# Kernel optimization log

Hardware: AMD Instinct MI355X
Metric: run time of the kernel (lower is better)

Reference implementation:

```python
import jax, jax.numpy as jnp
import numpy as np

B, N, C, L, E = 8, 8192, 256, 4, 131072  # graphs, nodes/graph, channels (in=hidden=out), layers, edges/graph


def setup_inputs() -> dict:
    key = jax.random.key(0)
    ks = jax.random.split(key, 9)
    batch_node_tsr = jax.random.normal(ks[0], (B, N, C), jnp.float32)
    edge_index = jax.random.randint(ks[1], (B, 2, E), 0, N, jnp.int32)
    batch_last_node_idx_list = jnp.arange(1, B + 1, dtype=jnp.int32) * N - 1
    s1 = 1.0 / np.sqrt(C)
    s2 = 1.0 / np.sqrt(2 * C)
    # Base GraphConv layers: out = x @ Wr.T + sum_nbr(x) @ Wn.T + b  (all CxC since in=hidden=out)
    base_Wr = jax.random.uniform(ks[2], (L, C, C), jnp.float32, -s1, s1)
    base_Wn = jax.random.uniform(ks[3], (L, C, C), jnp.float32, -s1, s1)
    base_b = jax.random.uniform(ks[4], (L, C), jnp.float32, -s1, s1)
    # Adapter GraphConv layers take concatenated (2C) input
    adapt_Wr = jax.random.uniform(ks[5], (L, C, 2 * C), jnp.float32, -s2, s2)
    adapt_Wn = jax.random.uniform(ks[6], (L, C, 2 * C), jnp.float32, -s2, s2)
    adapt_b = jax.random.uniform(ks[7], (L, C), jnp.float32, -s2, s2)
    return dict(batch_node_tsr=batch_node_tsr, base_Wr=base_Wr, base_Wn=base_Wn,
                base_b=base_b, adapt_Wr=adapt_Wr, adapt_Wn=adapt_Wn, adapt_b=adapt_b,
                edge_index=edge_index, batch_last_node_idx_list=batch_last_node_idx_list)


def reference(batch_node_tsr, base_Wr, base_Wn, base_b, adapt_Wr, adapt_Wn, adapt_b,
              edge_index, batch_last_node_idx_list):
    # Batch graphs PyG-style: offset per-graph node indices into one big graph
    offsets = (jnp.arange(B, dtype=edge_index.dtype) * N)[:, None]  # [B,1]
    src = (edge_index[:, 0, :] + offsets).reshape(-1)  # [B*E]
    dst = (edge_index[:, 1, :] + offsets).reshape(-1)  # [B*E]
    x = batch_node_tsr.reshape(B * N, C)

    def gconv(h, Wr, Wn, b):
        # GraphConv: root transform + sum-aggregated neighbor transform
        agg = jax.ops.segment_sum(h[src], dst, num_segments=B * N)
        return h @ Wr.T + agg @ Wn.T + b

    # Base encoder pass, keeping all latent embeds
    lat = [x]
    for i in range(L):
        lat.append(jax.nn.relu(gconv(lat[-1], base_Wr[i], base_Wn[i], base_b[i])))
    base_batch_embed = lat[-1].reshape(B, N, C)

    # Adapter pass: concat(base_latent[i+1], curr) -> adapter GraphConv -> relu
    curr = x
    for i in range(L):
        curr = jax.nn.relu(gconv(jnp.concatenate([lat[i + 1], curr], axis=-1),
                                 adapt_Wr[i], adapt_Wn[i], adapt_b[i]))
    adapter_batch_embed = curr.reshape(B, N, C)
    return base_batch_embed, adapter_batch_embed
```

## Files before the change

### kernel.cpp

```cpp
#include <hip/hip_runtime.h>

#define B_ 8
#define N_ 8192
#define C_ 256
#define L_ 4
#define E_ 131072
#define BN_ 65536
#define EDGES_ 1048576

typedef __attribute__((ext_vector_type(8))) short short8;
typedef __attribute__((ext_vector_type(4))) float f32x4;

__device__ __forceinline__ unsigned short f2bf(float f){
  unsigned int u = __builtin_bit_cast(unsigned int, f);
  u += 0x7fffu + ((u >> 16) & 1u);
  return (unsigned short)(u >> 16);
}
__device__ __forceinline__ float bf2f(unsigned short h){
  unsigned int u = ((unsigned int)h) << 16;
  return __builtin_bit_cast(float, u);
}

__launch_bounds__(256)
__global__ void cvt_bf16_k(const float* __restrict__ in, unsigned short* __restrict__ out, int n4){
  int t = blockIdx.x * 256 + threadIdx.x;
  if (t >= n4) return;
  float4 v = ((const float4*)in)[t];
  ushort4 o;
  o.x = f2bf(v.x); o.y = f2bf(v.y); o.z = f2bf(v.z); o.w = f2bf(v.w);
  ((ushort4*)out)[t] = o;
}

__launch_bounds__(256)
__global__ void hist_k(const int* __restrict__ ei, int* __restrict__ cnt){
  int t = blockIdx.x * 256 + threadIdx.x;
  int b = t >> 17, e = t & (E_ - 1);
  int dst = ei[b * (2 * E_) + E_ + e];
  atomicAdd(&cnt[(b << 13) + dst], 1);
}

__launch_bounds__(256)
__global__ void scan_k(const int* __restrict__ cnt, int* __restrict__ row_ptr, int* __restrict__ cursor){
  __shared__ int lsum[256];
  int t = threadIdx.x;
  int base = t << 8;
  int s = 0;
  for (int i = 0; i < 256; ++i) s += cnt[base + i];
  lsum[t] = s;
  __syncthreads();
  for (int d = 1; d < 256; d <<= 1){
    int v = (t >= d) ? lsum[t - d] : 0;
    __syncthreads();
    lsum[t] += v;
    __syncthreads();
  }
  int off = lsum[t] - s;
  for (int i = 0; i < 256; ++i){
    row_ptr[base + i] = off;
    cursor[base + i]  = off;
    off += cnt[base + i];
  }
  if (t == 255) row_ptr[BN_] = off;
}

__launch_bounds__(256)
__global__ void scat_k(const int* __restrict__ ei, int* __restrict__ cursor, int* __restrict__ col){
  int t = blockIdx.x * 256 + threadIdx.x;
  int b = t >> 17, e = t & (E_ - 1);
  int src = ei[b * (2 * E_) + e];
  int dst = ei[b * (2 * E_) + E_ + e];
  int pos = atomicAdd(&cursor[(b << 13) + dst], 1);
  col[pos] = (b << 13) + src;
}

__launch_bounds__(256)
__global__ void agg_k(const unsigned short* __restrict__ feat, const int* __restrict__ row_ptr,
                      const int* __restrict__ col, unsigned short* __restrict__ out){
  int w = threadIdx.x >> 6, lane = threadIdx.x & 63;
  int g = blockIdx.x & 7, sblk = blockIdx.x >> 3;
  int node = (g << 13) + (sblk << 2) + w;
  int beg = row_ptr[node], end = row_ptr[node + 1];
  int ch = lane << 2;
  float a0=0,a1=0,a2=0,a3=0,b0=0,b1=0,b2=0,b3=0;
  int e = beg;
  for (; e + 2 <= end; e += 2){
    int s0 = col[e], s1 = col[e + 1];
    ushort4 v0 = *(const ushort4*)(feat + ((size_t)s0 << 8) + ch);
    ushort4 v1 = *(const ushort4*)(feat + ((size_t)s1 << 8) + ch);
    a0 += bf2f(v0.x); a1 += bf2f(v0.y); a2 += bf2f(v0.z); a3 += bf2f(v0.w);
    b0 += bf2f(v1.x); b1 += bf2f(v1.y); b2 += bf2f(v1.z); b3 += bf2f(v1.w);
  }
  if (e < end){
    int s0 = col[e];
    ushort4 v0 = *(const ushort4*)(feat + ((size_t)s0 << 8) + ch);
    a0 += bf2f(v0.x); a1 += bf2f(v0.y); a2 += bf2f(v0.z); a3 += bf2f(v0.w);
  }
  ushort4 o;
  o.x = f2bf(a0 + b0); o.y = f2bf(a1 + b1); o.z = f2bf(a2 + b2); o.w = f2bf(a3 + b3);
  *(ushort4*)(out + ((size_t)node << 8) + ch) = o;
}

__launch_bounds__(256)
__global__ void agg2_k(const unsigned short* __restrict__ fA, const unsigned short* __restrict__ fB,
                       const int* __restrict__ row_ptr, const int* __restrict__ col,
                       unsigned short* __restrict__ oA, unsigned short* __restrict__ oB){
  int w = threadIdx.x >> 6, lane = threadIdx.x & 63;
  int g = blockIdx.x & 7, sblk = blockIdx.x >> 3;
  int node = (g << 13) + (sblk << 2) + w;
  int beg = row_ptr[node], end = row_ptr[node + 1];
  int ch = lane << 2;
  float a0=0,a1=0,a2=0,a3=0, c0=0,c1=0,c2=0,c3=0;
  float a4=0,a5=0,a6=0,a7=0, c4=0,c5=0,c6=0,c7=0;
  int e = beg;
  for (; e + 2 <= end; e += 2){
    int s0 = col[e], s1 = col[e + 1];
    ushort4 va0 = *(const ushort4*)(fA + ((size_t)s0 << 8) + ch);
    ushort4 vb0 = *(const ushort4*)(fB + ((size_t)s0 << 8) + ch);
    ushort4 va1 = *(const ushort4*)(fA + ((size_t)s1 << 8) + ch);
    ushort4 vb1 = *(const ushort4*)(fB + ((size_t)s1 << 8) + ch);
    a0 += bf2f(va0.x); a1 += bf2f(va0.y); a2 += bf2f(va0.z); a3 += bf2f(va0.w);
    c0 += bf2f(vb0.x); c1 += bf2f(vb0.y); c2 += bf2f(vb0.z); c3 += bf2f(vb0.w);
    a4 += bf2f(va1.x); a5 += bf2f(va1.y); a6 += bf2f(va1.z); a7 += bf2f(va1.w);
    c4 += bf2f(vb1.x); c5 += bf2f(vb1.y); c6 += bf2f(vb1.z); c7 += bf2f(vb1.w);
  }
  if (e < end){
    int s0 = col[e];
    ushort4 va0 = *(const ushort4*)(fA + ((size_t)s0 << 8) + ch);
    ushort4 vb0 = *(const ushort4*)(fB + ((size_t)s0 << 8) + ch);
    a0 += bf2f(va0.x); a1 += bf2f(va0.y); a2 += bf2f(va0.z); a3 += bf2f(va0.w);
    c0 += bf2f(vb0.x); c1 += bf2f(vb0.y); c2 += bf2f(vb0.z); c3 += bf2f(vb0.w);
  }
  ushort4 oa, ob;
  oa.x = f2bf(a0 + a4); oa.y = f2bf(a1 + a5); oa.z = f2bf(a2 + a6); oa.w = f2bf(a3 + a7);
  ob.x = f2bf(c0 + c4); ob.y = f2bf(c1 + c5); ob.z = f2bf(c2 + c6); ob.w = f2bf(c3 + c7);
  *(ushort4*)(oA + ((size_t)node << 8) + ch) = oa;
  *(ushort4*)(oB + ((size_t)node << 8) + ch) = ob;
}

#define GLDS16(gp, lp) __builtin_amdgcn_global_load_lds( \
    (const __attribute__((address_space(1))) void*)(gp), \
    (__attribute__((address_space(3))) void*)(lp), 16, 0, 0)

template<int P>
__launch_bounds__(256)
__global__ void gemm_k(const unsigned short* __restrict__ A0, const unsigned short* __restrict__ A1,
                       const unsigned short* __restrict__ A2, const unsigned short* __restrict__ A3,
                       const unsigned short* __restrict__ W0, const unsigned short* __restrict__ W1,
                       const unsigned short* __restrict__ W2, const unsigned short* __restrict__ W3,
                       int ldw, const float* __restrict__ bias,
                       unsigned short* __restrict__ outb, float* __restrict__ outf){
  __shared__ unsigned short lds_u[12288];
  unsigned short* a_t = lds_u;
  unsigned short* b_t = lds_u + 4096;
  const unsigned short* As[4] = {A0, A1, A2, A3};
  const unsigned short* Ws[4] = {W0, W1, W2, W3};
  const int m0 = blockIdx.x << 7;
  const int t = threadIdx.x, lane = t & 63;
  const int w = t >> 6;
  const int lrow = lane & 15, kg = lane >> 4;
  f32x4 acc[2][16] = {};
#pragma unroll
  for (int p = 0; p < P; ++p){
    const unsigned short* A = As[p] + (size_t)m0 * C_;
    const unsigned short* W = Ws[p];
    for (int k0 = 0; k0 < C_; k0 += 32){
#pragma unroll
      for (int c = t; c < 512; c += 256){
        int row = c >> 2, seg = c & 3;
        GLDS16(A + row * C_  + k0 + seg * 8, &a_t[c * 8]);
      }
#pragma unroll
      for (int c = t; c < 1024; c += 256){
        int row = c >> 2, seg = c & 3;
        GLDS16(W + row * ldw + k0 + seg * 8, &b_t[c * 8]);
      }
      __syncthreads();
      short8 af[2];
#pragma unroll
      for (int m = 0; m < 2; ++m)
        af[m] = *(const short8*)&a_t[((w << 5) + (m << 4) + lrow) * 32 + (kg << 3)];
#pragma unroll
      for (int h = 0; h < 2; ++h){
        short8 bfr[8];
#pragma unroll
        for (int n2 = 0; n2 < 8; ++n2)
          bfr[n2] = *(const short8*)&b_t[((h << 7) + (n2 << 4) + lrow) * 32 + (kg << 3)];
#pragma unroll
        for (int m = 0; m < 2; ++m)
#pragma unroll
          for (int n2 = 0; n2 < 8; ++n2)
            acc[m][(h << 3) + n2] =
                __builtin_amdgcn_mfma_f32_16x16x32_bf16(af[m], bfr[n2], acc[m][(h << 3) + n2], 0, 0, 0);
      }
      __syncthreads();
    }
  }
  float bv[16];
#pragma unroll
  for (int n = 0; n < 16; ++n) bv[n] = bias[(n << 4) + lrow];
  unsigned short* ep = lds_u + (w << 11);
#pragma unroll
  for (int m = 0; m < 2; ++m){
    const int gr = m0 + (w << 5) + (m << 4);
    if (outf){
#pragma unroll
      for (int n = 0; n < 16; ++n)
#pragma unroll
        for (int j = 0; j < 4; ++j){
          float v = acc[m][n][j] + bv[n];
          v = v > 0.f ? v : 0.f;
          outf[(size_t)(gr + (kg << 2) + j) * C_ + (n << 4) + lrow] = v;
        }
    }
    if (outb){
#pragma unroll
      for (int h = 0; h < 2; ++h){
#pragma unroll
        for (int n2 = 0; n2 < 8; ++n2){
          int n = (h << 3) + n2;
#pragma unroll
          for (int j = 0; j < 4; ++j){
            float v = acc[m][n][j] + bv[n];
            v = v > 0.f ? v : 0.f;
            ep[((kg << 2) + j) * 128 + (n2 << 4) + lrow] = f2bf(v);
          }
        }
#pragma unroll
        for (int k = 0; k < 4; ++k){
          int r = (lane >> 4) + (k << 2);
          short8 v = *(const short8*)&ep[r * 128 + (lane & 15) * 8];
          *(short8*)&outb[(size_t)(gr + r) * C_ + (h << 7) + (lane & 15) * 8] = v;
        }
      }
    }
  }
}

extern "C" void kernel_launch(void* const* d_in, const int* in_sizes, int n_in,
                              void* d_out, int out_size, void* d_ws, size_t ws_size,
                              hipStream_t stream){
  const float* x_f   = (const float*)d_in[0];
  const float* bWr_f = (const float*)d_in[1];
  const float* bWn_f = (const float*)d_in[2];
  const float* bB    = (const float*)d_in[3];
  const float* aWr_f = (const float*)d_in[4];
  const float* aWn_f = (const float*)d_in[5];
  const float* aB    = (const float*)d_in[6];
  const int*   ei    = (const int*)d_in[7];
  float* out = (float*)d_out;
  (void)in_sizes; (void)n_in; (void)out_size; (void)ws_size;

  char* p = (char*)d_ws;
  const size_t BUF = (size_t)BN_ * C_ * sizeof(unsigned short);
  auto alloc = [&](size_t bytes){ void* r = (void*)p; p += (bytes + 255) & ~(size_t)255; return r; };
  unsigned short* xb   = (unsigned short*)alloc(BUF);
  unsigned short* latA = (unsigned short*)alloc(BUF);
  unsigned short* latB = (unsigned short*)alloc(BUF);
  unsigned short* curA = (unsigned short*)alloc(BUF);
  unsigned short* curB = (unsigned short*)alloc(BUF);
  unsigned short* agg0 = (unsigned short*)alloc(BUF);
  unsigned short* agg1 = (unsigned short*)alloc(BUF);
  unsigned short* wbR  = (unsigned short*)alloc((size_t)L_ * C_ * C_ * 2);
  unsigned short* wbN  = (unsigned short*)alloc((size_t)L_ * C_ * C_ * 2);
  unsigned short* waR  = (unsigned short*)alloc((size_t)L_ * C_ * 2 * C_ * 2);
  unsigned short* waN  = (unsigned short*)alloc((size_t)L_ * C_ * 2 * C_ * 2);
  int* cnt     = (int*)alloc((size_t)BN_ * 4);
  int* row_ptr = (int*)alloc((size_t)(BN_ + 1) * 4);
  int* cursor  = (int*)alloc((size_t)BN_ * 4);
  int* colx    = (int*)alloc((size_t)EDGES_ * 4);

  cvt_bf16_k<<<BN_ * C_ / 4 / 256, 256, 0, stream>>>(x_f, xb, BN_ * C_ / 4);
  cvt_bf16_k<<<L_ * C_ * C_ / 4 / 256, 256, 0, stream>>>(bWr_f, wbR, L_ * C_ * C_ / 4);
  cvt_bf16_k<<<L_ * C_ * C_ / 4 / 256, 256, 0, stream>>>(bWn_f, wbN, L_ * C_ * C_ / 4);
  cvt_bf16_k<<<L_ * C_ * 2 * C_ / 4 / 256, 256, 0, stream>>>(aWr_f, waR, L_ * C_ * 2 * C_ / 4);
  cvt_bf16_k<<<L_ * C_ * 2 * C_ / 4 / 256, 256, 0, stream>>>(aWn_f, waN, L_ * C_ * 2 * C_ / 4);

  hipMemsetAsync(cnt, 0, (size_t)BN_ * 4, stream);
  hist_k<<<EDGES_ / 256, 256, 0, stream>>>(ei, cnt);
  scan_k<<<1, 256, 0, stream>>>(cnt, row_ptr, cursor);
  scat_k<<<EDGES_ / 256, 256, 0, stream>>>(ei, cursor, colx);

  const int AGG_GRID  = BN_ / 4;
  const int GEMM_GRID = BN_ / 128;

  const size_t WB = (size_t)C_ * C_;
  const size_t WA = (size_t)C_ * 2 * C_;

  agg_k<<<AGG_GRID, 256, 0, stream>>>(xb, row_ptr, colx, agg0);
  gemm_k<2><<<GEMM_GRID, 256, 0, stream>>>(xb, agg0, nullptr, nullptr,
      wbR, wbN, nullptr, nullptr, C_, bB, latA, nullptr);
  agg_k<<<AGG_GRID, 256, 0, stream>>>(latA, row_ptr, colx, agg1);
  gemm_k<2><<<GEMM_GRID, 256, 0, stream>>>(latA, agg1, nullptr, nullptr,
      wbR + WB, wbN + WB, nullptr, nullptr, C_, bB + 256, latB, nullptr);
  gemm_k<4><<<GEMM_GRID, 256, 0, stream>>>(latA, xb, agg1, agg0,
      waR, waR + 256, waN, waN + 256, 2 * C_, aB, curA, nullptr);
  agg2_k<<<AGG_GRID, 256, 0, stream>>>(latB, curA, row_ptr, colx, agg1, agg0);
  gemm_k<2><<<GEMM_GRID, 256, 0, stream>>>(latB, agg1, nullptr, nullptr,
      wbR + 2 * WB, wbN + 2 * WB, nullptr, nullptr, C_, bB + 512, latA, nullptr);
  gemm_k<4><<<GEMM_GRID, 256, 0, stream>>>(latB, curA, agg1, agg0,
      waR + WA, waR + WA + 256, waN + WA, waN + WA + 256, 2 * C_, aB + 256, curB, nullptr);
  agg2_k<<<AGG_GRID, 256, 0, stream>>>(latA, curB, row_ptr, colx, agg1, agg0);
  gemm_k<2><<<GEMM_GRID, 256, 0, stream>>>(latA, agg1, nullptr, nullptr,
      wbR + 3 * WB, wbN + 3 * WB, nullptr, nullptr, C_, bB + 768, latB, out);
  gemm_k<4><<<GEMM_GRID, 256, 0, stream>>>(latA, curB, agg1, agg0,
      waR + 2 * WA, waR + 2 * WA + 256, waN + 2 * WA, waN + 2 * WA + 256, 2 * C_, aB + 512, curA, nullptr);
  agg2_k<<<AGG_GRID, 256, 0, stream>>>(latB, curA, row_ptr, colx, agg1, agg0);
  gemm_k<4><<<GEMM_GRID, 256, 0, stream>>>(latB, curA, agg1, agg0,
      waR + 3 * WA, waR + 3 * WA + 256, waN + 3 * WA, waN + 3 * WA + 256, 2 * C_, aB + 768,
      nullptr, out + (size_t)BN_ * C_);
}
```

Baseline: 1.248 ms.

## Double-buffer GEMM LDS tiles, bucket CSR by source range, stage fp32 epilogue

The GEMM now double-buffers its LDS tiles so the next k-slice's global-to-LDS loads overlap MFMA work on the current slice, using one barrier per step. The CSR build keys edges by destination plus a 2-bit source-range bucket, so each node's neighbors are partially sorted by source for better gather locality. The aggregation loops unroll by four. The fp32 output epilogue is staged through LDS to issue coalesced float4 stores. Costs are double the LDS use (lower occupancy), a four-times larger count/scan array handled by a single-block scan, and extra LDS traffic in the epilogue.

```diff
diff --git a/kernel.cpp b/kernel.cpp
--- a/kernel.cpp
+++ b/kernel.cpp
@@ -7,6 +7,7 @@
 #define E_ 131072
 #define BN_ 65536
 #define EDGES_ 1048576
+#define NKEY_ (BN_ * 4)
 
 typedef __attribute__((ext_vector_type(8))) short short8;
 typedef __attribute__((ext_vector_type(4))) float f32x4;
@@ -35,17 +36,21 @@
 __global__ void hist_k(const int* __restrict__ ei, int* __restrict__ cnt){
   int t = blockIdx.x * 256 + threadIdx.x;
   int b = t >> 17, e = t & (E_ - 1);
+  int src = ei[b * (2 * E_) + e];
   int dst = ei[b * (2 * E_) + E_ + e];
-  atomicAdd(&cnt[(b << 13) + dst], 1);
+  int key = (((b << 13) + dst) << 2) | (src >> 11);
+  atomicAdd(&cnt[key], 1);
 }
 
 __launch_bounds__(256)
 __global__ void scan_k(const int* __restrict__ cnt, int* __restrict__ row_ptr, int* __restrict__ cursor){
   __shared__ int lsum[256];
   int t = threadIdx.x;
-  int base = t << 8;
+  const int CH = NKEY_ / 256;
+  int base = t * CH;
   int s = 0;
-  for (int i = 0; i < 256; ++i) s += cnt[base + i];
+  const int4* c4 = (const int4*)(cnt + base);
+  for (int i = 0; i < CH / 4; ++i){ int4 v = c4[i]; s += v.x + v.y + v.z + v.w; }
   lsum[t] = s;
   __syncthreads();
   for (int d = 1; d < 256; d <<= 1){
@@ -55,12 +60,12 @@
     __syncthreads();
   }
   int off = lsum[t] - s;
-  for (int i = 0; i < 256; ++i){
+  for (int i = 0; i < CH; ++i){
     row_ptr[base + i] = off;
     cursor[base + i]  = off;
     off += cnt[base + i];
   }
-  if (t == 255) row_ptr[BN_] = off;
+  if (t == 255) row_ptr[NKEY_] = off;
 }
 
 __launch_bounds__(256)
@@ -69,7 +74,8 @@
   int b = t >> 17, e = t & (E_ - 1);
   int src = ei[b * (2 * E_) + e];
   int dst = ei[b * (2 * E_) + E_ + e];
-  int pos = atomicAdd(&cursor[(b << 13) + dst], 1);
+  int key = (((b << 13) + dst) << 2) | (src >> 11);
+  int pos = atomicAdd(&cursor[key], 1);
   col[pos] = (b << 13) + src;
 }
 
@@ -79,24 +85,28 @@
   int w = threadIdx.x >> 6, lane = threadIdx.x & 63;
   int g = blockIdx.x & 7, sblk = blockIdx.x >> 3;
   int node = (g << 13) + (sblk << 2) + w;
-  int beg = row_ptr[node], end = row_ptr[node + 1];
+  int beg = row_ptr[node << 2], end = row_ptr[(node << 2) + 4];
   int ch = lane << 2;
-  float a0=0,a1=0,a2=0,a3=0,b0=0,b1=0,b2=0,b3=0;
+  float a0=0,a1=0,a2=0,a3=0;
   int e = beg;
-  for (; e + 2 <= end; e += 2){
-    int s0 = col[e], s1 = col[e + 1];
+  for (; e + 4 <= end; e += 4){
+    int s0 = col[e], s1 = col[e+1], s2 = col[e+2], s3 = col[e+3];
     ushort4 v0 = *(const ushort4*)(feat + ((size_t)s0 << 8) + ch);
     ushort4 v1 = *(const ushort4*)(feat + ((size_t)s1 << 8) + ch);
-    a0 += bf2f(v0.x); a1 += bf2f(v0.y); a2 += bf2f(v0.z); a3 += bf2f(v0.w);
-    b0 += bf2f(v1.x); b1 += bf2f(v1.y); b2 += bf2f(v1.z); b3 += bf2f(v1.w);
-  }
-  if (e < end){
+    ushort4 v2 = *(const ushort4*)(feat + ((size_t)s2 << 8) + ch);
+    ushort4 v3 = *(const ushort4*)(feat + ((size_t)s3 << 8) + ch);
+    a0 += (bf2f(v0.x) + bf2f(v1.x)) + (bf2f(v2.x) + bf2f(v3.x));
+    a1 += (bf2f(v0.y) + bf2f(v1.y)) + (bf2f(v2.y) + bf2f(v3.y));
+    a2 += (bf2f(v0.z) + bf2f(v1.z)) + (bf2f(v2.z) + bf2f(v3.z));
+    a3 += (bf2f(v0.w) + bf2f(v1.w)) + (bf2f(v2.w) + bf2f(v3.w));
+  }
+  for (; e < end; ++e){
     int s0 = col[e];
     ushort4 v0 = *(const ushort4*)(feat + ((size_t)s0 << 8) + ch);
     a0 += bf2f(v0.x); a1 += bf2f(v0.y); a2 += bf2f(v0.z); a3 += bf2f(v0.w);
   }
   ushort4 o;
-  o.x = f2bf(a0 + b0); o.y = f2bf(a1 + b1); o.z = f2bf(a2 + b2); o.w = f2bf(a3 + b3);
+  o.x = f2bf(a0); o.y = f2bf(a1); o.z = f2bf(a2); o.w = f2bf(a3);
   *(ushort4*)(out + ((size_t)node << 8) + ch) = o;
 }
 
@@ -107,23 +117,30 @@
   int w = threadIdx.x >> 6, lane = threadIdx.x & 63;
   int g = blockIdx.x & 7, sblk = blockIdx.x >> 3;
   int node = (g << 13) + (sblk << 2) + w;
-  int beg = row_ptr[node], end = row_ptr[node + 1];
+  int beg = row_ptr[node << 2], end = row_ptr[(node << 2) + 4];
   int ch = lane << 2;
   float a0=0,a1=0,a2=0,a3=0, c0=0,c1=0,c2=0,c3=0;
-  float a4=0,a5=0,a6=0,a7=0, c4=0,c5=0,c6=0,c7=0;
   int e = beg;
-  for (; e + 2 <= end; e += 2){
-    int s0 = col[e], s1 = col[e + 1];
+  for (; e + 4 <= end; e += 4){
+    int s0 = col[e], s1 = col[e+1], s2 = col[e+2], s3 = col[e+3];
     ushort4 va0 = *(const ushort4*)(fA + ((size_t)s0 << 8) + ch);
+    ushort4 va1 = *(const ushort4*)(fA + ((size_t)s1 << 8) + ch);
+    ushort4 va2 = *(const ushort4*)(fA + ((size_t)s2 << 8) + ch);
+    ushort4 va3 = *(const ushort4*)(fA + ((size_t)s3 << 8) + ch);
     ushort4 vb0 = *(const ushort4*)(fB + ((size_t)s0 << 8) + ch);
-    ushort4 va1 = *(const ushort4*)(fA + ((size_t)s1 << 8) + ch);
     ushort4 vb1 = *(const ushort4*)(fB + ((size_t)s1 << 8) + ch);
-    a0 += bf2f(va0.x); a1 += bf2f(va0.y); a2 += bf2f(va0.z); a3 += bf2f(va0.w);
-    c0 += bf2f(vb0.x); c1 += bf2f(vb0.y); c2 += bf2f(vb0.z); c3 += bf2f(vb0.w);
-    a4 += bf2f(va1.x); a5 += bf2f(va1.y); a6 += bf2f(va1.z); a7 += bf2f(va1.w);
-    c4 += bf2f(vb1.x); c5 += bf2f(vb1.y); c6 += bf2f(vb1.z); c7 += bf2f(vb1.w);
-  }
-  if (e < end){
+    ushort4 vb2 = *(const ushort4*)(fB + ((size_t)s2 << 8) + ch);
+    ushort4 vb3 = *(const ushort4*)(fB + ((size_t)s3 << 8) + ch);
+    a0 += (bf2f(va0.x) + bf2f(va1.x)) + (bf2f(va2.x) + bf2f(va3.x));
+    a1 += (bf2f(va0.y) + bf2f(va1.y)) + (bf2f(va2.y) + bf2f(va3.y));
+    a2 += (bf2f(va0.z) + bf2f(va1.z)) + (bf2f(va2.z) + bf2f(va3.z));
+    a3 += (bf2f(va0.w) + bf2f(va1.w)) + (bf2f(va2.w) + bf2f(va3.w));
+    c0 += (bf2f(vb0.x) + bf2f(vb1.x)) + (bf2f(vb2.x) + bf2f(vb3.x));
+    c1 += (bf2f(vb0.y) + bf2f(vb1.y)) + (bf2f(vb2.y) + bf2f(vb3.y));
+    c2 += (bf2f(vb0.z) + bf2f(vb1.z)) + (bf2f(vb2.z) + bf2f(vb3.z));
+    c3 += (bf2f(vb0.w) + bf2f(vb1.w)) + (bf2f(vb2.w) + bf2f(vb3.w));
+  }
+  for (; e < end; ++e){
     int s0 = col[e];
     ushort4 va0 = *(const ushort4*)(fA + ((size_t)s0 << 8) + ch);
     ushort4 vb0 = *(const ushort4*)(fB + ((size_t)s0 << 8) + ch);
@@ -131,8 +148,8 @@
     c0 += bf2f(vb0.x); c1 += bf2f(vb0.y); c2 += bf2f(vb0.z); c3 += bf2f(vb0.w);
   }
   ushort4 oa, ob;
-  oa.x = f2bf(a0 + a4); oa.y = f2bf(a1 + a5); oa.z = f2bf(a2 + a6); oa.w = f2bf(a3 + a7);
-  ob.x = f2bf(c0 + c4); ob.y = f2bf(c1 + c5); ob.z = f2bf(c2 + c6); ob.w = f2bf(c3 + c7);
+  oa.x = f2bf(a0); oa.y = f2bf(a1); oa.z = f2bf(a2); oa.w = f2bf(a3);
+  ob.x = f2bf(c0); ob.y = f2bf(c1); ob.z = f2bf(c2); ob.w = f2bf(c3);
   *(ushort4*)(oA + ((size_t)node << 8) + ch) = oa;
   *(ushort4*)(oB + ((size_t)node << 8) + ch) = ob;
 }
@@ -149,9 +166,7 @@
                        const unsigned short* __restrict__ W2, const unsigned short* __restrict__ W3,
                        int ldw, const float* __restrict__ bias,
                        unsigned short* __restrict__ outb, float* __restrict__ outf){
-  __shared__ unsigned short lds_u[12288];
-  unsigned short* a_t = lds_u;
-  unsigned short* b_t = lds_u + 4096;
+  __shared__ unsigned short lds_u[24576];
   const unsigned short* As[4] = {A0, A1, A2, A3};
   const unsigned short* Ws[4] = {W0, W1, W2, W3};
   const int m0 = blockIdx.x << 7;
@@ -159,58 +174,98 @@
   const int w = t >> 6;
   const int lrow = lane & 15, kg = lane >> 4;
   f32x4 acc[2][16] = {};
+  int cur = 0;
+
 #pragma unroll
   for (int p = 0; p < P; ++p){
     const unsigned short* A = As[p] + (size_t)m0 * C_;
     const unsigned short* W = Ws[p];
-    for (int k0 = 0; k0 < C_; k0 += 32){
+    {
+      unsigned short* a_t = lds_u + cur * 12288;
+      unsigned short* b_t = a_t + 4096;
 #pragma unroll
       for (int c = t; c < 512; c += 256){
         int row = c >> 2, seg = c & 3;
-        GLDS16(A + row * C_  + k0 + seg * 8, &a_t[c * 8]);
+        GLDS16(A + row * C_  + seg * 8, &a_t[c * 8]);
       }
 #pragma unroll
       for (int c = t; c < 1024; c += 256){
         int row = c >> 2, seg = c & 3;
-        GLDS16(W + row * ldw + k0 + seg * 8, &b_t[c * 8]);
-      }
-      __syncthreads();
-      short8 af[2];
-#pragma unroll
-      for (int m = 0; m < 2; ++m)
-        af[m] = *(const short8*)&a_t[((w << 5) + (m << 4) + lrow) * 32 + (kg << 3)];
-#pragma unroll
-      for (int h = 0; h < 2; ++h){
-        short8 bfr[8];
-#pragma unroll
-        for (int n2 = 0; n2 < 8; ++n2)
-          bfr[n2] = *(const short8*)&b_t[((h << 7) + (n2 << 4) + lrow) * 32 + (kg << 3)];
+        GLDS16(W + row * ldw + seg * 8, &b_t[c * 8]);
+      }
+      asm volatile("s_waitcnt vmcnt(0)" ::: "memory");
+      __builtin_amdgcn_s_barrier();
+    }
+    for (int ks = 0; ks < 8; ++ks){
+      if (ks < 7){
+        int k0 = (ks + 1) << 5;
+        unsigned short* a_t = lds_u + (cur ^ 1) * 12288;
+        unsigned short* b_t = a_t + 4096;
+#pragma unroll
+        for (int c = t; c < 512; c += 256){
+          int row = c >> 2, seg = c & 3;
+          GLDS16(A + row * C_  + k0 + seg * 8, &a_t[c * 8]);
+        }
+#pragma unroll
+        for (int c = t; c < 1024; c += 256){
+          int row = c >> 2, seg = c & 3;
+          GLDS16(W + row * ldw + k0 + seg * 8, &b_t[c * 8]);
+        }
+      }
+      {
+        const unsigned short* a_t = lds_u + cur * 12288;
+        const unsigned short* b_t = a_t + 4096;
+        short8 af[2];
 #pragma unroll
         for (int m = 0; m < 2; ++m)
+          af[m] = *(const short8*)&a_t[((w << 5) + (m << 4) + lrow) * 32 + (kg << 3)];
+#pragma unroll
+        for (int h = 0; h < 2; ++h){
+          short8 bfr[8];
 #pragma unroll
           for (int n2 = 0; n2 < 8; ++n2)
-            acc[m][(h << 3) + n2] =
-                __builtin_amdgcn_mfma_f32_16x16x32_bf16(af[m], bfr[n2], acc[m][(h << 3) + n2], 0, 0, 0);
-      }
-      __syncthreads();
+            bfr[n2] = *(const short8*)&b_t[((h << 7) + (n2 << 4) + lrow) * 32 + (kg << 3)];
+#pragma unroll
+          for (int m = 0; m < 2; ++m)
+#pragma unroll
+            for (int n2 = 0; n2 < 8; ++n2)
+              acc[m][(h << 3) + n2] =
+                  __builtin_amdgcn_mfma_f32_16x16x32_bf16(af[m], bfr[n2], acc[m][(h << 3) + n2], 0, 0, 0);
+        }
+      }
+      asm volatile("s_waitcnt vmcnt(0)" ::: "memory");
+      __builtin_amdgcn_s_barrier();
+      cur ^= 1;
     }
   }
   float bv[16];
 #pragma unroll
   for (int n = 0; n < 16; ++n) bv[n] = bias[(n << 4) + lrow];
-  unsigned short* ep = lds_u + (w << 11);
+  unsigned short* ep  = lds_u + (w << 11);
+  float*          epf = (float*)(&lds_u[8192]) + (w << 11);
 #pragma unroll
   for (int m = 0; m < 2; ++m){
     const int gr = m0 + (w << 5) + (m << 4);
     if (outf){
 #pragma unroll
-      for (int n = 0; n < 16; ++n)
-#pragma unroll
-        for (int j = 0; j < 4; ++j){
-          float v = acc[m][n][j] + bv[n];
-          v = v > 0.f ? v : 0.f;
-          outf[(size_t)(gr + (kg << 2) + j) * C_ + (n << 4) + lrow] = v;
-        }
+      for (int h = 0; h < 2; ++h){
+#pragma unroll
+        for (int n2 = 0; n2 < 8; ++n2){
+          int n = (h << 3) + n2;
+#pragma unroll
+          for (int j = 0; j < 4; ++j){
+            float v = acc[m][n][j] + bv[n];
+            v = v > 0.f ? v : 0.f;
+            epf[((kg << 2) + j) * 128 + (n2 << 4) + lrow] = v;
+          }
+        }
+#pragma unroll
+        for (int k = 0; k < 8; ++k){
+          int r = (lane >> 5) + (k << 1);
+          float4 v = *(const float4*)&epf[r * 128 + (lane & 31) * 4];
+          *(float4*)&outf[(size_t)(gr + r) * C_ + (h << 7) + (lane & 31) * 4] = v;
+        }
+      }
     }
     if (outb){
 #pragma unroll
@@ -264,9 +319,9 @@
   unsigned short* wbN  = (unsigned short*)alloc((size_t)L_ * C_ * C_ * 2);
   unsigned short* waR  = (unsigned short*)alloc((size_t)L_ * C_ * 2 * C_ * 2);
   unsigned short* waN  = (unsigned short*)alloc((size_t)L_ * C_ * 2 * C_ * 2);
-  int* cnt     = (int*)alloc((size_t)BN_ * 4);
-  int* row_ptr = (int*)alloc((size_t)(BN_ + 1) * 4);
-  int* cursor  = (int*)alloc((size_t)BN_ * 4);
+  int* cnt     = (int*)alloc((size_t)NKEY_ * 4);
+  int* row_ptr = (int*)alloc((size_t)(NKEY_ + 1) * 4);
+  int* cursor  = (int*)alloc((size_t)NKEY_ * 4);
   int* colx    = (int*)alloc((size_t)EDGES_ * 4);
 
   cvt_bf16_k<<<BN_ * C_ / 4 / 256, 256, 0, stream>>>(x_f, xb, BN_ * C_ / 4);
@@ -275,7 +330,7 @@
   cvt_bf16_k<<<L_ * C_ * 2 * C_ / 4 / 256, 256, 0, stream>>>(aWr_f, waR, L_ * C_ * 2 * C_ / 4);
   cvt_bf16_k<<<L_ * C_ * 2 * C_ / 4 / 256, 256, 0, stream>>>(aWn_f, waN, L_ * C_ * 2 * C_ / 4);
 
-  hipMemsetAsync(cnt, 0, (size_t)BN_ * 4, stream);
+  hipMemsetAsync(cnt, 0, (size_t)NKEY_ * 4, stream);
   hist_k<<<EDGES_ / 256, 256, 0, stream>>>(ei, cnt);
   scan_k<<<1, 256, 0, stream>>>(cnt, row_ptr, cursor);
   scat_k<<<EDGES_ / 256, 256, 0, stream>>>(ei, cursor, colx);
```

New measurement: 1.234 ms. About the same (-1.2%).
